# Optimization experiments

Hardware: AMD Instinct MI355X
Metric: run time of the kernel (lower is better)

The kernel has to match this reference:

```python
import jax, jax.numpy as jnp
import numpy as np

B, T_IN, T_OUT, V, C = 2048, 10, 25, 22, 3
D = V * C            # embed / gru hidden = 66
H = 3                # attention heads
HD = D // H          # head dim = 22
EPS = 1e-5
DIMS = [(C, 64), (64, 32), (32, 64), (64, C)]


def _bn(x, g, b):
    # eval-mode BatchNorm2d with default running stats (mean=0, var=1)
    return x * (g / jnp.sqrt(1.0 + EPS))[None, :, None, None] + b[None, :, None, None]


def _gcn_layer(x, A, Tm, cw, cb, g, bt, rw, rb, rg, rbt, pre):
    # x: (N, Cin, T, V); STSGCN ST_GCNN_layer with 1x1 conv (kernel [1,1])
    res = _bn(jnp.einsum('nctv,oc->notv', x, rw) + rb[None, :, None, None], rg, rbt)
    y = jnp.einsum('nctv,vtq->ncqv', x, Tm)   # temporal mixing
    y = jnp.einsum('nctv,tvw->nctw', y, A)    # spatial (joint) mixing
    y = _bn(jnp.einsum('nctv,oc->notv', y, cw) + cb[None, :, None, None], g, bt)
    y = y + res
    return jnp.where(y >= 0, y, pre * y)      # PReLU (scalar slope)


def setup_inputs() -> dict:
    key = jax.random.key(0)
    ks = iter(jax.random.split(key, 64))
    def rn(shape, s=0.05):
        return jax.random.normal(next(ks), shape, dtype=jnp.float32) * s
    d = {"x": rn((B, T_IN, V, C), 1.0)}
    d["A"] = rn((4, T_IN, V, V), 0.2)
    d["Tm"] = rn((4, V, T_IN, T_IN), 0.3)
    d["pre"] = jnp.full((4,), 0.25, jnp.float32)
    for i, (ci, co) in enumerate(DIMS):
        d[f"cw{i}"] = rn((co, ci), 0.1)
        d[f"cb{i}"] = rn((co,), 0.1)
        d[f"g{i}"] = jnp.ones((co,), jnp.float32)
        d[f"bt{i}"] = jnp.zeros((co,), jnp.float32)
        d[f"rw{i}"] = rn((co, ci), 0.1)
        d[f"rb{i}"] = rn((co,), 0.1)
        d[f"rg{i}"] = jnp.ones((co,), jnp.float32)
        d[f"rbt{i}"] = jnp.zeros((co,), jnp.float32)
    d["gru_wi"] = rn((3 * D, D)); d["gru_wh"] = rn((3 * D, D))
    d["gru_bi"] = rn((3 * D,));   d["gru_bh"] = rn((3 * D,))
    d["qkv_w"] = rn((3 * D, D)); d["qkv_b"] = rn((3 * D,))
    d["ow"] = rn((D, D)); d["ob"] = rn((D,))
    d["lw"] = rn((D, 2 * D)); d["lb"] = rn((D,))
    return d


def _forward(x, A, Tm, pre, cws, cbs, gs, bts, rws, rbs, rgs, rbts,
             gru_wi, gru_wh, gru_bi, gru_bh, qkv_w, qkv_b, ow, ob, lw, lb):
    raw = x.reshape(B, T_IN, D)                 # (N,T,V*C), joint-major flatten
    h = jnp.transpose(x, (0, 3, 1, 2))          # (N,C,T,V)
    for i in range(4):
        h = _gcn_layer(h, A[i], Tm[i], cws[i], cbs[i], gs[i], bts[i],
                       rws[i], rbs[i], rgs[i], rbts[i], pre[i])
    enc = jnp.transpose(h, (0, 2, 3, 1)).reshape(B, T_IN, D)  # (N,T,V*C)

    wq, wk, wv = qkv_w[:D], qkv_w[D:2 * D], qkv_w[2 * D:]
    bq, bk, bv = qkv_b[:D], qkv_b[D:2 * D], qkv_b[2 * D:]
    # K,V of encoder sequence are constant across decode steps: project once
    k = (enc @ wk.T + bk).reshape(B, T_IN, H, HD)
    v = (enc @ wv.T + bv).reshape(B, T_IN, H, HD)
    scale = 1.0 / jnp.sqrt(jnp.float32(HD))

    def gru(inp, hprev):
        gi = inp @ gru_wi.T + gru_bi
        gh = hprev @ gru_wh.T + gru_bh
        ir, iz, inn = jnp.split(gi, 3, axis=-1)
        hr, hz, hn = jnp.split(gh, 3, axis=-1)
        r = jax.nn.sigmoid(ir + hr)
        z = jax.nn.sigmoid(iz + hz)
        n = jnp.tanh(inn + r * hn)
        return (1.0 - z) * n + z * hprev

    def step(carry, _):
        hs, tp = carry
        hs = gru(tp, hs)
        q = ((hs @ wq.T + bq) * scale).reshape(B, H, HD)
        scores = jnp.einsum('bhd,bthd->bht', q, k)
        attn = jax.nn.softmax(scores, axis=-1)
        ctx = jnp.einsum('bht,bthd->bhd', attn, v).reshape(B, D) @ ow.T + ob
        pred = jnp.concatenate([hs, ctx], axis=-1) @ lw.T + lb + tp  # residual
        return (hs, pred), pred

    h0 = enc[:, -1, :]
    tp0 = raw[:, -1, :]
    _, preds = jax.lax.scan(step, (h0, tp0), None, length=T_OUT)
    out = jnp.transpose(preds, (1, 0, 2))       # (N, T_out, D)
    return out.reshape(B, T_OUT, V, C)


def reference(x, A, Tm, pre,
              cw0, cb0, g0, bt0, rw0, rb0, rg0, rbt0,
              cw1, cb1, g1, bt1, rw1, rb1, rg1, rbt1,
              cw2, cb2, g2, bt2, rw2, rb2, rg2, rbt2,
              cw3, cb3, g3, bt3, rw3, rb3, rg3, rbt3,
              gru_wi, gru_wh, gru_bi, gru_bh, qkv_w, qkv_b, ow, ob, lw, lb):
    return _forward(x, A, Tm, pre,
                    [cw0, cw1, cw2, cw3], [cb0, cb1, cb2, cb3],
                    [g0, g1, g2, g3], [bt0, bt1, bt2, bt3],
                    [rw0, rw1, rw2, rw3], [rb0, rb1, rb2, rb3],
                    [rg0, rg1, rg2, rg3], [rbt0, rbt1, rbt2, rbt3],
                    gru_wi, gru_wh, gru_bi, gru_bh, qkv_w, qkv_b, ow, ob, lw, lb)
```

## Files before the change

### kernel.cpp

```cpp
#include <hip/hip_runtime.h>

#define DEV static __device__ __forceinline__


struct EncW {
  const float* cw[4]; const float* cb[4]; const float* g[4]; const float* bt[4];
  const float* rw[4]; const float* rb[4]; const float* rg[4]; const float* rbt[4];
};


template<int CI, int CO, int OGRAN>
DEV void gcn_orig(int tid,
    const float* __restrict__ cw, const float* __restrict__ cb,
    const float* __restrict__ gg, const float* __restrict__ bt,
    const float* __restrict__ rw, const float* __restrict__ rb,
    const float* __restrict__ rg, const float* __restrict__ rbt,
    const float* __restrict__ TmL, const float* __restrict__ AL, float preL,
    float* __restrict__ act, float* __restrict__ S,
    float* __restrict__ rmul, float* __restrict__ radd,
    float* __restrict__ cmul, float* __restrict__ cadd)
{
  constexpr int COP8 = (CO + 7) & ~7;
  constexpr int NT = (CO / OGRAN) * 55;
  constexpr int RWN = CI * COP8;
  static_assert(RWN + 2200 <= 4840, "rw+Tm co-stage must fit in S");
  const float inv = 0.99999499987f;

  for (int idx = tid; idx < RWN + 2200; idx += 512) {
    if (idx < RWN) {
      int c = idx / COP8, o = idx % COP8;
      S[idx] = (o < CO) ? rw[o * CI + c] : 0.f;
    } else {
      int j = idx - RWN;
      int tq = j / 22, v = j % 22;
      S[idx] = TmL[v * 100 + tq];
    }
  }
  for (int idx = tid; idx < 64; idx += 512) {
    bool ok = idx < CO;
    float rm = ok ? rg[idx] * inv : 0.f;
    float cm = ok ? gg[idx] * inv : 0.f;
    rmul[idx] = rm;
    radd[idx] = ok ? rb[idx] * rm + rbt[idx] : 0.f;
    cmul[idx] = cm;
    cadd[idx] = ok ? cb[idx] * cm + bt[idx] : 0.f;
  }
  __syncthreads();

  float racc[OGRAN * 4];
  const int og = tid / 55, pp = tid % 55;
  if (tid < NT) {
    #pragma unroll
    for (int k = 0; k < OGRAN * 4; ++k) racc[k] = 0.f;
    #pragma unroll 4
    for (int c = 0; c < CI; ++c) {
      const float* wr = S + c * COP8 + og * OGRAN;
      float4 av = *(const float4*)(act + c * 220 + pp * 4);
      float wv[OGRAN];
      if constexpr (OGRAN == 8) {
        float4 w0 = *(const float4*)(wr);
        float4 w1 = *(const float4*)(wr + 4);
        wv[0]=w0.x; wv[1]=w0.y; wv[2]=w0.z; wv[3]=w0.w;
        wv[4]=w1.x; wv[5]=w1.y; wv[6]=w1.z; wv[7]=w1.w;
      } else if constexpr (OGRAN == 4) {
        float4 w0 = *(const float4*)(wr);
        wv[0]=w0.x; wv[1]=w0.y; wv[2]=w0.z; wv[3]=w0.w;
      } else {
        wv[0] = wr[0];
      }
      #pragma unroll
      for (int o = 0; o < OGRAN; ++o) {
        racc[o*4+0] += wv[o]*av.x; racc[o*4+1] += wv[o]*av.y;
        racc[o*4+2] += wv[o]*av.z; racc[o*4+3] += wv[o]*av.w;
      }
    }
    #pragma unroll
    for (int o = 0; o < OGRAN; ++o) {
      float m = rmul[og * OGRAN + o], a = radd[og * OGRAN + o];
      #pragma unroll
      for (int k = 0; k < 4; ++k) racc[o*4+k] = racc[o*4+k]*m + a;
    }
  }
  __syncthreads();

  for (int idx = tid; idx < CI * 11; idx += 512) {
    int v2 = idx % 11, c = idx / 11;
    float* base = act + c * 220 + v2 * 2;
    float xin[10][2];
    #pragma unroll
    for (int t = 0; t < 10; ++t) { xin[t][0] = base[t*22]; xin[t][1] = base[t*22+1]; }
    float ya[10][2];
    #pragma unroll
    for (int q = 0; q < 10; ++q) { ya[q][0] = 0.f; ya[q][1] = 0.f; }
    #pragma unroll
    for (int t = 0; t < 10; ++t) {
      const float* tm = S + RWN + t * 220 + v2 * 2;
      #pragma unroll
      for (int q = 0; q < 10; ++q) {
        ya[q][0] += tm[q*22]   * xin[t][0];
        ya[q][1] += tm[q*22+1] * xin[t][1];
      }
    }
    #pragma unroll
    for (int q = 0; q < 10; ++q) { base[q*22] = ya[q][0]; base[q*22+1] = ya[q][1]; }
  }
  __syncthreads();

  for (int idx = tid; idx < 4840; idx += 512) S[idx] = AL[idx];
  __syncthreads();

  for (int idx = tid; idx < CI * 10; idx += 512) {
    int t = idx % 10, c = idx / 10;
    float* row = act + c * 220 + t * 22;
    float yin[22];
    #pragma unroll
    for (int v = 0; v < 22; ++v) yin[v] = row[v];
    float za[22];
    #pragma unroll
    for (int w = 0; w < 22; ++w) za[w] = 0.f;
    #pragma unroll 2
    for (int v = 0; v < 22; ++v) {
      const float* ar = S + (t * 22 + v) * 22;
      float y0 = yin[v];
      #pragma unroll
      for (int w = 0; w < 22; ++w) za[w] += y0 * ar[w];
    }
    #pragma unroll
    for (int w = 0; w < 22; ++w) row[w] = za[w];
  }
  __syncthreads();

  for (int idx = tid; idx < RWN; idx += 512) {
    int c = idx / COP8, o = idx % COP8;
    S[idx] = (o < CO) ? cw[o * CI + c] : 0.f;
  }
  __syncthreads();

  float cacc[OGRAN * 4];
  if (tid < NT) {
    #pragma unroll
    for (int k = 0; k < OGRAN * 4; ++k) cacc[k] = 0.f;
    #pragma unroll 4
    for (int c = 0; c < CI; ++c) {
      const float* wr = S + c * COP8 + og * OGRAN;
      float4 av = *(const float4*)(act + c * 220 + pp * 4);
      float wv[OGRAN];
      if constexpr (OGRAN == 8) {
        float4 w0 = *(const float4*)(wr);
        float4 w1 = *(const float4*)(wr + 4);
        wv[0]=w0.x; wv[1]=w0.y; wv[2]=w0.z; wv[3]=w0.w;
        wv[4]=w1.x; wv[5]=w1.y; wv[6]=w1.z; wv[7]=w1.w;
      } else if constexpr (OGRAN == 4) {
        float4 w0 = *(const float4*)(wr);
        wv[0]=w0.x; wv[1]=w0.y; wv[2]=w0.z; wv[3]=w0.w;
      } else {
        wv[0] = wr[0];
      }
      #pragma unroll
      for (int o = 0; o < OGRAN; ++o) {
        cacc[o*4+0] += wv[o]*av.x; cacc[o*4+1] += wv[o]*av.y;
        cacc[o*4+2] += wv[o]*av.z; cacc[o*4+3] += wv[o]*av.w;
      }
    }
  }
  __syncthreads();
  if (tid < NT) {
    #pragma unroll
    for (int o = 0; o < OGRAN; ++o) {
      float m = cmul[og * OGRAN + o], a = cadd[og * OGRAN + o];
      #pragma unroll
      for (int k = 0; k < 4; ++k) {
        float y = cacc[o*4+k]*m + a + racc[o*4+k];
        act[(og*OGRAN+o)*220 + pp*4 + k] = (y >= 0.f) ? y : preL * y;
      }
    }
  }
  __syncthreads();
}

template<int CI, int CO, int OGRAN>
DEV void gcn_reord(int tid,
    const float* __restrict__ cw, const float* __restrict__ cb,
    const float* __restrict__ gg, const float* __restrict__ bt,
    const float* __restrict__ rw, const float* __restrict__ rb,
    const float* __restrict__ rg, const float* __restrict__ rbt,
    const float* __restrict__ TmL, const float* __restrict__ AL, float preL,
    float* __restrict__ act, float* __restrict__ S,
    float* __restrict__ rmul, float* __restrict__ radd,
    float* __restrict__ cmul, float* __restrict__ cadd)
{
  constexpr int CO2 = 2 * CO;
  constexpr int COP8 = (CO2 + 7) & ~7;
  constexpr int NT = (CO2 / OGRAN) * 55;
  constexpr int RWN = CI * COP8;
  static_assert(RWN <= 4840, "W2 must fit in S");
  const float inv = 0.99999499987f;

  for (int idx = tid; idx < RWN; idx += 512) {
    int c = idx / COP8, o = idx % COP8;
    float w = 0.f;
    if (o < CO) w = cw[o * CI + c];
    else if (o < CO2) w = rw[(o - CO) * CI + c];
    S[idx] = w;
  }
  for (int idx = tid; idx < 64; idx += 512) {
    bool ok = idx < CO;
    float rm = ok ? rg[idx] * inv : 0.f;
    float cm = ok ? gg[idx] * inv : 0.f;
    rmul[idx] = rm;
    radd[idx] = ok ? rb[idx] * rm + rbt[idx] : 0.f;
    cmul[idx] = cm;
    cadd[idx] = ok ? cb[idx] * cm + bt[idx] : 0.f;
  }
  __syncthreads();

  float acc[OGRAN * 4];
  const int og = tid / 55, pp = tid % 55;
  if (tid < NT) {
    #pragma unroll
    for (int k = 0; k < OGRAN * 4; ++k) acc[k] = 0.f;
    #pragma unroll 4
    for (int c = 0; c < CI; ++c) {
      const float* wr = S + c * COP8 + og * OGRAN;
      float4 av = *(const float4*)(act + c * 220 + pp * 4);
      float wv[OGRAN];
      if constexpr (OGRAN == 8) {
        float4 w0 = *(const float4*)(wr);
        float4 w1 = *(const float4*)(wr + 4);
        wv[0]=w0.x; wv[1]=w0.y; wv[2]=w0.z; wv[3]=w0.w;
        wv[4]=w1.x; wv[5]=w1.y; wv[6]=w1.z; wv[7]=w1.w;
      } else if constexpr (OGRAN == 4) {
        float4 w0 = *(const float4*)(wr);
        wv[0]=w0.x; wv[1]=w0.y; wv[2]=w0.z; wv[3]=w0.w;
      } else {
        wv[0] = wr[0];
      }
      #pragma unroll
      for (int o = 0; o < OGRAN; ++o) {
        acc[o*4+0] += wv[o]*av.x; acc[o*4+1] += wv[o]*av.y;
        acc[o*4+2] += wv[o]*av.z; acc[o*4+3] += wv[o]*av.w;
      }
    }
  }
  __syncthreads();

  if (tid < NT) {
    #pragma unroll
    for (int o = 0; o < OGRAN; ++o) {
      const int oo = og * OGRAN + o;
      const bool isr = oo >= CO;
      const float m = isr ? rmul[oo - CO] : 1.f;
      const float a = isr ? radd[oo - CO] : 0.f;
      #pragma unroll
      for (int k = 0; k < 4; ++k)
        act[oo * 220 + pp * 4 + k] = acc[o*4+k] * m + a;
    }
  }
  for (int i = tid; i < 2200; i += 512) {
    int tq = i / 22, v = i % 22;
    S[i] = TmL[v * 100 + tq];
  }
  __syncthreads();

  for (int idx = tid; idx < CO * 11; idx += 512) {
    int v2 = idx % 11, c = idx / 11;
    float* base = act + c * 220 + v2 * 2;
    float xin[10][2];
    #pragma unroll
    for (int t = 0; t < 10; ++t) { xin[t][0] = base[t*22]; xin[t][1] = base[t*22+1]; }
    float ya[10][2];
    #pragma unroll
    for (int q = 0; q < 10; ++q) { ya[q][0] = 0.f; ya[q][1] = 0.f; }
    #pragma unroll
    for (int t = 0; t < 10; ++t) {
      const float* tm = S + t * 220 + v2 * 2;
      #pragma unroll
      for (int q = 0; q < 10; ++q) {
        ya[q][0] += tm[q*22]   * xin[t][0];
        ya[q][1] += tm[q*22+1] * xin[t][1];
      }
    }
    #pragma unroll
    for (int q = 0; q < 10; ++q) { base[q*22] = ya[q][0]; base[q*22+1] = ya[q][1]; }
  }
  __syncthreads();

  for (int idx = tid; idx < 4840; idx += 512) S[idx] = AL[idx];
  __syncthreads();

  for (int idx = tid; idx < CO * 10; idx += 512) {
    int t = idx % 10, c = idx / 10;
    float* row = act + c * 220 + t * 22;
    float yin[22];
    #pragma unroll
    for (int v = 0; v < 22; ++v) yin[v] = row[v];
    float za[22];
    #pragma unroll
    for (int w = 0; w < 22; ++w) za[w] = 0.f;
    #pragma unroll 2
    for (int v = 0; v < 22; ++v) {
      const float* ar = S + (t * 22 + v) * 22;
      float y0 = yin[v];
      #pragma unroll
      for (int w = 0; w < 22; ++w) za[w] += y0 * ar[w];
    }
    #pragma unroll
    for (int w = 0; w < 22; ++w) row[w] = za[w];
  }
  __syncthreads();

  for (int idx = tid; idx < CO * 220; idx += 512) {
    int o = idx / 220, p = idx % 220;
    float y = act[o * 220 + p] * cmul[o] + cadd[o] + act[(CO + o) * 220 + p];
    act[o * 220 + p] = (y >= 0.f) ? y : preL * y;
  }
  __syncthreads();
}

__global__ __launch_bounds__(512, 4)
void enc_kernel(const float* __restrict__ x, const float* __restrict__ A,
                const float* __restrict__ Tm, const float* __restrict__ pre, EncW W,
                const float* __restrict__ qkvT, const float* __restrict__ qkv_b,
                float* __restrict__ h0_ws, float* __restrict__ k_ws,
                float* __restrict__ v_ws)
{
  __shared__ __align__(16) float act[64 * 220];
  __shared__ __align__(16) float S[4840];
  __shared__ float rmul[64], radd[64], cmul[64], cadd[64];

  const int tid = threadIdx.x;
  const int b = blockIdx.x;

  for (int idx = tid; idx < 660; idx += 512) {
    int c = idx / 220, r = idx % 220, t = r / 22, v = r % 22;
    act[c * 220 + t * 22 + v] = x[(((size_t)b * 10 + t) * 22 + v) * 3 + c];
  }
  float p0 = pre[0], p1 = pre[1], p2 = pre[2], p3 = pre[3];

  gcn_orig<3, 64, 8>(tid, W.cw[0], W.cb[0], W.g[0], W.bt[0], W.rw[0], W.rb[0], W.rg[0], W.rbt[0],
                     Tm, A, p0, act, S, rmul, radd, cmul, cadd);
  gcn_reord<64, 32, 8>(tid, W.cw[1], W.cb[1], W.g[1], W.bt[1], W.rw[1], W.rb[1], W.rg[1], W.rbt[1],
                     Tm + 2200, A + 4840, p1, act, S, rmul, radd, cmul, cadd);
  gcn_orig<32, 64, 8>(tid, W.cw[2], W.cb[2], W.g[2], W.bt[2], W.rw[2], W.rb[2], W.rg[2], W.rbt[2],
                     Tm + 4400, A + 9680, p2, act, S, rmul, radd, cmul, cadd);
  gcn_reord<64, 3, 1>(tid, W.cw[3], W.cb[3], W.g[3], W.bt[3], W.rw[3], W.rb[3], W.rg[3], W.rbt[3],
                     Tm + 6600, A + 14520, p3, act, S, rmul, radd, cmul, cadd);

  float* encD = act + 3 * 220;
  for (int idx = tid; idx < 660; idx += 512) {
    int t = idx / 66, d = idx % 66, v = d / 3, c = d % 3;
    float val = act[c * 220 + t * 22 + v];
    encD[idx] = val;
    if (t == 9) h0_ws[(size_t)b * 66 + d] = val;
  }
  __syncthreads();

  for (int idx = tid; idx < 1320; idx += 512) {
    const int t = idx / 132, dd = idx % 132;
    const int row = 66 + dd;
    const float* wp = qkvT + row;
    const float* ep = encD + t * 66;
    float acc = 0.f;
    #pragma unroll 6
    for (int e = 0; e < 66; ++e) acc += wp[e * 198] * ep[e];
    acc += qkv_b[row];
    const int half = dd / 66, d = dd - half * 66;
    float* dst = half ? v_ws : k_ws;
    dst[(size_t)b * 660 + t * 66 + d] = acc;
  }
}


__global__ __launch_bounds__(512)
void prep_kernel(const float* __restrict__ qkv_w, const float* __restrict__ ow,
                 const float* __restrict__ ob, const float* __restrict__ lw,
                 const float* __restrict__ gru_wi, const float* __restrict__ gru_wh,
                 float* __restrict__ qkvT, float* __restrict__ wqD,
                 float* __restrict__ lwAT, float* __restrict__ MT,
                 float* __restrict__ cb2, float* __restrict__ wT_g)
{
  int idx = blockIdx.x * 512 + threadIdx.x;
  if (idx < 13068) {
    int e = idx / 198, j = idx % 198;
    qkvT[idx] = qkv_w[j * 66 + e];
    return;
  }
  int i1 = idx - 13068;
  if (i1 < 4356) {
    int e = i1 / 66, d = i1 % 66;
    wqD[i1] = qkv_w[d * 66 + e];
    return;
  }
  int i2 = i1 - 4356;
  if (i2 < 4356) {
    int e = i2 / 66, d = i2 % 66;
    lwAT[i2] = lw[d * 132 + e];
    return;
  }
  int i3 = i2 - 4356;
  if (i3 < 4356) {
    int e = i3 / 66, d = i3 % 66;
    const float* lrow = lw + d * 132 + 66;
    float acc = 0.f;
    for (int f = 0; f < 66; ++f) acc += lrow[f] * ow[f * 66 + e];
    MT[i3] = acc;
    return;
  }
  int i4 = i3 - 4356;
  if (i4 < 66) {
    const float* lrow = lw + i4 * 132 + 66;
    float acc = 0.f;
    for (int f = 0; f < 66; ++f) acc += lrow[f] * ob[f];
    cb2[i4] = acc;
    return;
  }
  int i5 = i4 - 66;
  if (i5 < 26136) {
    int e = i5 / 396, jm = i5 % 396;
    wT_g[i5] = (jm < 198) ? gru_wi[jm * 66 + e] : gru_wh[(jm - 198) * 66 + e];
  }
}


__global__ __launch_bounds__(512, 4)
void dec_kernel(const float* __restrict__ x, const float* __restrict__ h0_ws,
                const float* __restrict__ k_ws, const float* __restrict__ v_ws,
                const float* __restrict__ wT_g,
                const float* __restrict__ gru_bi, const float* __restrict__ gru_bh,
                const float* __restrict__ wqD, const float* __restrict__ qkv_b,
                const float* __restrict__ lwAT, const float* __restrict__ MT,
                const float* __restrict__ cb2, const float* __restrict__ lb,
                float* __restrict__ outp)
{
  __shared__ __align__(16) float wqS[4356];
  __shared__ __align__(16) float lwAS[4356];
  __shared__ __align__(16) float MS[4356];
  __shared__ __align__(16) float kS[2640];
  __shared__ __align__(16) float G[396 * 4];
  __shared__ __align__(16) float tpT[264], hsT[264], qT[264], cxT[264];
  __shared__ float attnS[120];
  __shared__ float biS[198], bhS[198], bqS[66], lbS[66];

  const int tid = threadIdx.x;
  const int b0 = blockIdx.x * 4;

  for (int idx = tid; idx < 4356; idx += 512) {
    wqS[idx] = wqD[idx]; lwAS[idx] = lwAT[idx]; MS[idx] = MT[idx];
  }
  for (int idx = tid; idx < 2640; idx += 512) {
    int r = idx / 660, rest = idx % 660;
    kS[idx] = k_ws[(size_t)(b0 + r) * 660 + rest];
  }
  for (int idx = tid; idx < 198; idx += 512) { biS[idx] = gru_bi[idx]; bhS[idx] = gru_bh[idx]; }
  for (int idx = tid; idx < 66; idx += 512)  { bqS[idx] = qkv_b[idx]; lbS[idx] = lb[idx] + cb2[idx]; }
  for (int idx = tid; idx < 264; idx += 512) {
    int d = idx >> 2, r = idx & 3;
    hsT[d * 4 + r] = h0_ws[(size_t)(b0 + r) * 66 + d];
    tpT[d * 4 + r] = x[(size_t)(b0 + r) * 660 + 594 + d];
  }
  __syncthreads();

  const float qscale = 1.0f / sqrtf(22.0f);

  for (int s = 0; s < 25; ++s) {
    if (tid < 396) {
      const float* base = (tid < 198) ? tpT : hsT;
      const float* wp = wT_g + tid;
      float a0 = 0.f, a1 = 0.f, a2 = 0.f, a3 = 0.f;
      #pragma unroll 11
      for (int e = 0; e < 66; ++e) {
        float w = wp[e * 396];
        float4 av = *(const float4*)(base + e * 4);
        a0 += w * av.x; a1 += w * av.y; a2 += w * av.z; a3 += w * av.w;
      }
      float bias = (tid < 198) ? biS[tid] : bhS[tid - 198];
      *(float4*)(G + tid * 4) = make_float4(a0 + bias, a1 + bias, a2 + bias, a3 + bias);
    }
    __syncthreads();

    if (tid < 264) {
      int d = tid >> 2, r = tid & 3;
      float ir = G[d * 4 + r]         + G[(198 + d) * 4 + r];
      float iz = G[(66 + d) * 4 + r]  + G[(264 + d) * 4 + r];
      float nx = G[(132 + d) * 4 + r];
      float hn = G[(330 + d) * 4 + r];
      float rg = 1.f / (1.f + __expf(-ir));
      float zg = 1.f / (1.f + __expf(-iz));
      float t2 = __expf(2.f * (nx + rg * hn));
      float ng = 1.f - 2.f / (t2 + 1.f);
      float h = hsT[d * 4 + r];
      hsT[d * 4 + r] = (1.f - zg) * ng + zg * h;
    }
    __syncthreads();

    if (tid < 264) {
      int r = tid / 66, d = tid % 66;
      float acc = 0.f;
      #pragma unroll 6
      for (int e = 0; e < 66; ++e)
        acc += wqS[e * 66 + d] * hsT[e * 4 + r];
      qT[d * 4 + r] = (acc + bqS[d]) * qscale;
    }
    __syncthreads();

    if (tid < 120) {
      int r = tid / 30, rem = tid % 30, h = rem / 10, t = rem % 10;
      const float* kp = kS + r * 660 + t * 66 + h * 22;
      const float* qp = qT + (h * 22) * 4 + r;
      float acc = 0.f;
      #pragma unroll
      for (int dd = 0; dd < 22; ++dd) acc += qp[dd * 4] * kp[dd];
      attnS[(r * 3 + h) * 10 + t] = acc;
    }
    __syncthreads();

    if (tid < 12) {
      float* sp = attnS + tid * 10;
      float mx = sp[0];
      #pragma unroll
      for (int t = 1; t < 10; ++t) mx = fmaxf(mx, sp[t]);
      float sum = 0.f;
      #pragma unroll
      for (int t = 0; t < 10; ++t) { float e = __expf(sp[t] - mx); sp[t] = e; sum += e; }
      float invs = 1.f / sum;
      #pragma unroll
      for (int t = 0; t < 10; ++t) sp[t] *= invs;
    }
    __syncthreads();

    if (tid < 264) {
      int r = tid / 66, d = tid % 66, h = d / 22;
      const float* ap = attnS + (r * 3 + h) * 10;
      const float* vp = v_ws + (size_t)(b0 + r) * 660 + d;
      float acc = 0.f;
      #pragma unroll
      for (int t = 0; t < 10; ++t) acc += ap[t] * vp[t * 66];
      cxT[d * 4 + r] = acc;
    }
    __syncthreads();

    if (tid < 264) {
      int r = tid / 66, d = tid % 66;
      float acc = 0.f;
      #pragma unroll 6
      for (int e = 0; e < 66; ++e)
        acc += lwAS[e * 66 + d] * hsT[e * 4 + r] + MS[e * 66 + d] * cxT[e * 4 + r];
      float pred = acc + lbS[d] + tpT[d * 4 + r];
      outp[((size_t)(b0 + r) * 25 + s) * 66 + d] = pred;
      tpT[d * 4 + r] = pred;
    }
    __syncthreads();
  }
}


extern "C" void kernel_launch(void* const* d_in, const int* in_sizes, int n_in,
                              void* d_out, int out_size, void* d_ws, size_t ws_size,
                              hipStream_t stream) {
  (void)in_sizes; (void)n_in; (void)out_size; (void)ws_size;
  const float* x   = (const float*)d_in[0];
  const float* A   = (const float*)d_in[1];
  const float* Tm  = (const float*)d_in[2];
  const float* pre = (const float*)d_in[3];
  EncW W;
  for (int i = 0; i < 4; ++i) {
    W.cw[i]  = (const float*)d_in[4 + 8 * i + 0];
    W.cb[i]  = (const float*)d_in[4 + 8 * i + 1];
    W.g[i]   = (const float*)d_in[4 + 8 * i + 2];
    W.bt[i]  = (const float*)d_in[4 + 8 * i + 3];
    W.rw[i]  = (const float*)d_in[4 + 8 * i + 4];
    W.rb[i]  = (const float*)d_in[4 + 8 * i + 5];
    W.rg[i]  = (const float*)d_in[4 + 8 * i + 6];
    W.rbt[i] = (const float*)d_in[4 + 8 * i + 7];
  }
  const float* gru_wi = (const float*)d_in[36];
  const float* gru_wh = (const float*)d_in[37];
  const float* gru_bi = (const float*)d_in[38];
  const float* gru_bh = (const float*)d_in[39];
  const float* qkv_w  = (const float*)d_in[40];
  const float* qkv_b  = (const float*)d_in[41];
  const float* ow     = (const float*)d_in[42];
  const float* ob     = (const float*)d_in[43];
  const float* lw     = (const float*)d_in[44];
  const float* lb     = (const float*)d_in[45];

  float* wsf  = (float*)d_ws;
  float* h0   = wsf;
  float* kw   = h0 + 2048 * 66;
  float* vw   = kw + 2048 * 660;
  float* qkvT = vw + 2048 * 660;
  float* wqD  = qkvT + 13068;
  float* lwAT = wqD + 4356;
  float* MT   = lwAT + 4356;
  float* cb2  = MT + 4356;
  float* wT_g = cb2 + 66;

  prep_kernel<<<103, 512, 0, stream>>>(qkv_w, ow, ob, lw, gru_wi, gru_wh,
                                       qkvT, wqD, lwAT, MT, cb2, wT_g);
  enc_kernel<<<2048, 512, 0, stream>>>(x, A, Tm, pre, W, qkvT, qkv_b, h0, kw, vw);
  dec_kernel<<<512, 512, 0, stream>>>(x, h0, kw, vw, wT_g, gru_bi, gru_bh,
                                      wqD, qkv_b, lwAT, MT, cb2, lb,
                                      (float*)d_out);
}
```

Baseline: 657.8 us.

## Fold query projection into keys and fuse softmax into context step

Precomputes, once per block, the product of the query weight matrix with the cached keys (plus a bias term), so each decoder step computes attention scores directly from the hidden state. This removes the per-step q projection and its barrier. The scores are now split across 480 threads with shuffle reductions, and the softmax is recomputed redundantly inside the context-accumulation threads, removing two more barriers. In exchange there is a larger up-front prologue (7920 dot products per block) and more shared memory for the projected keys.

```diff
diff --git a/kernel.cpp b/kernel.cpp
--- a/kernel.cpp
+++ b/kernel.cpp
@@ -432,35 +432,48 @@
                 const float* __restrict__ cb2, const float* __restrict__ lb,
                 float* __restrict__ outp)
 {
-  __shared__ __align__(16) float wqS[4356];
+  __shared__ __align__(16) float kpS[7920];
   __shared__ __align__(16) float lwAS[4356];
   __shared__ __align__(16) float MS[4356];
-  __shared__ __align__(16) float kS[2640];
   __shared__ __align__(16) float G[396 * 4];
-  __shared__ __align__(16) float tpT[264], hsT[264], qT[264], cxT[264];
+  __shared__ __align__(16) float tpT[264], hsT[264], cxT[264];
   __shared__ float attnS[120];
-  __shared__ float biS[198], bhS[198], bqS[66], lbS[66];
+  __shared__ float kbS[120];
+  __shared__ float biS[198], bhS[198], lbS[66];
 
   const int tid = threadIdx.x;
   const int b0 = blockIdx.x * 4;
+  const float qscale = 1.0f / sqrtf(22.0f);
 
   for (int idx = tid; idx < 4356; idx += 512) {
-    wqS[idx] = wqD[idx]; lwAS[idx] = lwAT[idx]; MS[idx] = MT[idx];
-  }
-  for (int idx = tid; idx < 2640; idx += 512) {
-    int r = idx / 660, rest = idx % 660;
-    kS[idx] = k_ws[(size_t)(b0 + r) * 660 + rest];
+    lwAS[idx] = lwAT[idx]; MS[idx] = MT[idx];
   }
   for (int idx = tid; idx < 198; idx += 512) { biS[idx] = gru_bi[idx]; bhS[idx] = gru_bh[idx]; }
-  for (int idx = tid; idx < 66; idx += 512)  { bqS[idx] = qkv_b[idx]; lbS[idx] = lb[idx] + cb2[idx]; }
+  for (int idx = tid; idx < 66; idx += 512)  { lbS[idx] = lb[idx] + cb2[idx]; }
   for (int idx = tid; idx < 264; idx += 512) {
     int d = idx >> 2, r = idx & 3;
     hsT[d * 4 + r] = h0_ws[(size_t)(b0 + r) * 66 + d];
     tpT[d * 4 + r] = x[(size_t)(b0 + r) * 660 + 594 + d];
   }
-  __syncthreads();
-
-  const float qscale = 1.0f / sqrtf(22.0f);
+  for (int idx = tid; idx < 7920; idx += 512) {
+    const int g = idx / 66, e = idx % 66;
+    const int r = g / 30, rem = g % 30, h = rem / 10, t = rem % 10;
+    const float* wq = wqD + e * 66 + h * 22;
+    const float* kv = k_ws + (size_t)(b0 + r) * 660 + t * 66 + h * 22;
+    float acc = 0.f;
+    #pragma unroll
+    for (int j = 0; j < 22; ++j) acc += wq[j] * kv[j];
+    kpS[idx] = acc * qscale;
+  }
+  for (int idx = tid; idx < 120; idx += 512) {
+    const int r = idx / 30, rem = idx % 30, h = rem / 10, t = rem % 10;
+    const float* kv = k_ws + (size_t)(b0 + r) * 660 + t * 66 + h * 22;
+    float acc = 0.f;
+    #pragma unroll
+    for (int j = 0; j < 22; ++j) acc += qkv_b[h * 22 + j] * kv[j];
+    kbS[idx] = acc * qscale;
+  }
+  __syncthreads();
 
   for (int s = 0; s < 25; ++s) {
     if (tid < 396) {
@@ -493,49 +506,36 @@
     }
     __syncthreads();
 
-    if (tid < 264) {
-      int r = tid / 66, d = tid % 66;
+    if (tid < 480) {
+      const int g = tid >> 2, q4 = tid & 3;
+      const int r = g / 30;
+      const int e0 = q4 * 17;
+      const int e1 = (q4 == 3) ? 66 : e0 + 17;
+      const float* kpr = kpS + g * 66;
       float acc = 0.f;
-      #pragma unroll 6
-      for (int e = 0; e < 66; ++e)
-        acc += wqS[e * 66 + d] * hsT[e * 4 + r];
-      qT[d * 4 + r] = (acc + bqS[d]) * qscale;
-    }
-    __syncthreads();
-
-    if (tid < 120) {
-      int r = tid / 30, rem = tid % 30, h = rem / 10, t = rem % 10;
-      const float* kp = kS + r * 660 + t * 66 + h * 22;
-      const float* qp = qT + (h * 22) * 4 + r;
-      float acc = 0.f;
-      #pragma unroll
-      for (int dd = 0; dd < 22; ++dd) acc += qp[dd * 4] * kp[dd];
-      attnS[(r * 3 + h) * 10 + t] = acc;
-    }
-    __syncthreads();
-
-    if (tid < 12) {
-      float* sp = attnS + tid * 10;
-      float mx = sp[0];
-      #pragma unroll
-      for (int t = 1; t < 10; ++t) mx = fmaxf(mx, sp[t]);
-      float sum = 0.f;
-      #pragma unroll
-      for (int t = 0; t < 10; ++t) { float e = __expf(sp[t] - mx); sp[t] = e; sum += e; }
-      float invs = 1.f / sum;
-      #pragma unroll
-      for (int t = 0; t < 10; ++t) sp[t] *= invs;
+      for (int e = e0; e < e1; ++e) acc += hsT[e * 4 + r] * kpr[e];
+      acc += __shfl_xor(acc, 1);
+      acc += __shfl_xor(acc, 2);
+      if (q4 == 0) attnS[g] = acc + kbS[g];
     }
     __syncthreads();
 
     if (tid < 264) {
       int r = tid / 66, d = tid % 66, h = d / 22;
-      const float* ap = attnS + (r * 3 + h) * 10;
+      const float* sp = attnS + (r * 3 + h) * 10;
+      float sc[10];
+      float mx = sp[0];
+      #pragma unroll
+      for (int t = 1; t < 10; ++t) { sc[t] = sp[t]; mx = fmaxf(mx, sp[t]); }
+      sc[0] = sp[0];
+      float sum = 0.f;
+      #pragma unroll
+      for (int t = 0; t < 10; ++t) { float e = __expf(sc[t] - mx); sc[t] = e; sum += e; }
       const float* vp = v_ws + (size_t)(b0 + r) * 660 + d;
       float acc = 0.f;
       #pragma unroll
-      for (int t = 0; t < 10; ++t) acc += ap[t] * vp[t * 66];
-      cxT[d * 4 + r] = acc;
+      for (int t = 0; t < 10; ++t) acc += sc[t] * vp[t * 66];
+      cxT[d * 4 + r] = acc / sum;
     }
     __syncthreads();
 
```

After: 661.2 us. Within noise of the previous version (+0.5%).
